# Kernel tuning notes

Hardware: AMD Instinct MI355X
Metric: run time of the kernel (lower is better)

The kernel has to match this reference:

```python
import jax, jax.numpy as jnp
import numpy as np

BH, N, D, M = 64, 8192, 64, 32


def _gaussian_orthogonal_random_matrix(nb_rows, nb_cols, rng):
    # faithful to torch version with scaling=0: QR-orthogonal rows scaled by
    # row norms of a gaussian matrix
    blocks = []
    rows_left = nb_rows
    while rows_left > 0:
        q, _ = np.linalg.qr(rng.standard_normal((nb_cols, nb_cols)))
        blocks.append(q.T[: min(rows_left, nb_cols)])
        rows_left -= nb_cols
    final = np.concatenate(blocks, axis=0)[:nb_rows]
    multiplier = np.linalg.norm(rng.standard_normal((nb_rows, nb_cols)), axis=1)
    return (multiplier[:, None] * final).astype(np.float32)


def setup_inputs() -> dict:
    key = jax.random.key(0)
    k1, k2, k3 = jax.random.split(key, 3)
    q = jax.random.normal(k1, (BH, N, D), dtype=jnp.float32)
    k = jax.random.normal(k2, (BH, N, D), dtype=jnp.float32)
    v = jax.random.normal(k3, (BH, N, D), dtype=jnp.float32)
    proj = jnp.asarray(_gaussian_orthogonal_random_matrix(M, D, np.random.default_rng(0)))
    return {"q": q, "k": k, "v": v, "proj": proj}


def _softmax_kernel(data, proj, is_query, eps=1e-4):
    d = data.shape[-1]
    data_normalizer = d ** -0.25
    ratio = proj.shape[0] ** -0.5
    # [bh, n, m] random-feature logits
    data_dash = jnp.einsum('bnd,md->bnm', data_normalizer * data, proj)
    diag = (0.5 * data_normalizer ** 2) * jnp.sum(data * data, axis=-1, keepdims=True)
    if is_query:
        mx = jnp.max(data_dash, axis=-1, keepdims=True)  # per-row max
    else:
        mx = jnp.max(data_dash)  # global max (as in torch.max(t) with no dim)
    return ratio * (jnp.exp(data_dash - diag - mx) + eps)


def reference(q, k, v, proj):
    qp = _softmax_kernel(q, proj, is_query=True)   # [bh, n, m]
    kp = _softmax_kernel(k, proj, is_query=False)  # [bh, n, m]
    # linear attention: k^T v aggregation then query contraction
    kv = jnp.einsum('bnm,bnd->bmd', kp, v)         # [bh, m, d]
    ksum = jnp.sum(kp, axis=1)                     # [bh, m]
    num = jnp.einsum('bnm,bmd->bnd', qp, kv)       # [bh, n, d]
    den = jnp.einsum('bnm,bm->bn', qp, ksum)       # [bh, n]
    return num / den[..., None]
```

## Files before the change

kernel.cpp:

```cpp
#include <hip/hip_runtime.h>
#include <math.h>

#define BH 64
#define NN 8192
#define DD 64
#define MM 32

#define NROWS (BH*NN)
#define NORMC 0.35355339059327379f
#define RATIO 0.17677669529663689f
#define EPSK  1e-4f
#define DIAGC 0.0625f

#define CPB 64
#define CHUNK 128
#define K12_BLOCKS (BH*CPB)

typedef __attribute__((ext_vector_type(8))) short short8;
typedef __attribute__((ext_vector_type(4))) float f32x4;

union FragU { uint4 u; short8 s; };

__device__ __forceinline__ unsigned bf16r(float x) {
  unsigned u = __float_as_uint(x);
  return (u + 0x7fffu + ((u >> 16) & 1u)) >> 16;
}
__device__ __forceinline__ void cvt8(const float* f, FragU& hi, FragU& lo) {
  unsigned h[8], lw[8];
  #pragma unroll
  for (int j = 0; j < 8; ++j) {
    h[j] = bf16r(f[j]);
    lw[j] = bf16r(f[j] - __uint_as_float(h[j] << 16));
  }
  hi.u = make_uint4(h[0]|(h[1]<<16),  h[2]|(h[3]<<16),  h[4]|(h[5]<<16),  h[6]|(h[7]<<16));
  lo.u = make_uint4(lw[0]|(lw[1]<<16), lw[2]|(lw[3]<<16), lw[4]|(lw[5]<<16), lw[6]|(lw[7]<<16));
}

#define MFMA(a,b,c) __builtin_amdgcn_mfma_f32_16x16x32_bf16((a),(b),(c),0,0,0)

__device__ __forceinline__ float wave_max(float v) {
  #pragma unroll
  for (int off = 32; off > 0; off >>= 1)
    v = fmaxf(v, __shfl_down(v, off, 64));
  return v;
}

__global__ void kfrag_proj(const float* __restrict__ proj,
                           uint4* __restrict__ pfH, uint4* __restrict__ pfL)
{
  const int t = threadIdx.x;
  const int l = t & 63, g = t >> 6;
  const int mt = g >> 1, ks = g & 1;
  const int lr = l & 15, lg = l >> 4;
  float f[8];
  #pragma unroll
  for (int j = 0; j < 8; ++j)
    f[j] = proj[(mt*16 + lr)*DD + ks*32 + lg*8 + j];
  FragU hi, lo; cvt8(f, hi, lo);
  pfH[g*64 + l] = hi.u;
  pfL[g*64 + l] = lo.u;
}

__global__ __launch_bounds__(256, 4) void k12_kv(
    const float* __restrict__ k, const float* __restrict__ v,
    const uint4* __restrict__ pfH, const uint4* __restrict__ pfL,
    float* __restrict__ kvPart, float* __restrict__ ksPart,
    float* __restrict__ vsPart, float* __restrict__ partialMax)
{
  __shared__ float red[8192];
  __shared__ float wmaxL[4];
  const int t = threadIdx.x;
  const int w = t >> 6, l = t & 63;
  const int lr = l & 15, lg = l >> 4;
  const int blk = blockIdx.x;
  const int b = blk >> 6, c = blk & (CPB - 1);
  const size_t nrow0 = (size_t)b * NN + (size_t)c * CHUNK + (size_t)w * 32;

  ushort* eh = (ushort*)red + w * 2560;
  ushort* el = eh + 1280;

  f32x4 accK[2][4];
  #pragma unroll
  for (int mt = 0; mt < 2; ++mt)
    #pragma unroll
    for (int dt = 0; dt < 4; ++dt)
      accK[mt][dt] = (f32x4){0.f, 0.f, 0.f, 0.f};
  float ksacc0 = 0.f, ksacc1 = 0.f;
  float vsum[4] = {0.f, 0.f, 0.f, 0.f};
  float tmax = -3.4e38f;

  #pragma unroll
  for (int rt = 0; rt < 2; ++rt) {
    float sq = 0.f;
    f32x4 a0 = {0.f,0.f,0.f,0.f}, a1 = {0.f,0.f,0.f,0.f};
    #pragma unroll
    for (int ks = 0; ks < 2; ++ks) {
      const float4* src = (const float4*)(k + (nrow0 + rt*16 + lr)*DD + ks*32 + lg*8);
      float4 x0 = src[0], x1 = src[1];
      float qv[8] = {x0.x,x0.y,x0.z,x0.w, x1.x,x1.y,x1.z,x1.w};
      #pragma unroll
      for (int j = 0; j < 8; ++j) sq += qv[j]*qv[j];
      FragU aH, aL; cvt8(qv, aH, aL);

      uintptr_t pfh_ = (uintptr_t)pfH, pfl_ = (uintptr_t)pfL;
      asm volatile("" : "+s"(pfh_), "+s"(pfl_));
      const uint4* pH = (const uint4*)pfh_;
      const uint4* pL = (const uint4*)pfl_;
      FragU pH0, pH1, pL0, pL1;
      pH0.u = pH[ks*64 + l];
      pH1.u = pH[(2+ks)*64 + l];
      pL0.u = pL[ks*64 + l];
      pL1.u = pL[(2+ks)*64 + l];

      a0 = MFMA(aL.s, pH0.s, a0);
      a0 = MFMA(aH.s, pL0.s, a0);
      a0 = MFMA(aH.s, pH0.s, a0);
      a1 = MFMA(aL.s, pH1.s, a1);
      a1 = MFMA(aH.s, pL1.s, a1);
      a1 = MFMA(aH.s, pH1.s, a1);
    }
    sq += __shfl_xor(sq, 16, 64);
    sq += __shfl_xor(sq, 32, 64);
    unsigned h0w[4], l0w[4], h1w[4], l1w[4];
    #pragma unroll
    for (int reg = 0; reg < 4; ++reg) {
      const float diag = DIAGC * __shfl(sq, lg*4 + reg, 64);
      const float d0 = a0[reg] * NORMC;
      const float d1 = a1[reg] * NORMC;
      tmax = fmaxf(tmax, fmaxf(d0, d1));
      const float e0 = __expf(d0 - diag);
      const float e1 = __expf(d1 - diag);
      ksacc0 += e0;
      ksacc1 += e1;
      h0w[reg] = bf16r(e0);
      l0w[reg] = bf16r(e0 - __uint_as_float(h0w[reg] << 16));
      h1w[reg] = bf16r(e1);
      l1w[reg] = bf16r(e1 - __uint_as_float(h1w[reg] << 16));
    }
    const int nloc = rt*16 + lg*4;
    *(unsigned*)(eh + lr*40      + nloc)     = h0w[0] | (h0w[1] << 16);
    *(unsigned*)(eh + lr*40      + nloc + 2) = h0w[2] | (h0w[3] << 16);
    *(unsigned*)(el + lr*40      + nloc)     = l0w[0] | (l0w[1] << 16);
    *(unsigned*)(el + lr*40      + nloc + 2) = l0w[2] | (l0w[3] << 16);
    *(unsigned*)(eh + (lr+16)*40 + nloc)     = h1w[0] | (h1w[1] << 16);
    *(unsigned*)(eh + (lr+16)*40 + nloc + 2) = h1w[2] | (h1w[3] << 16);
    *(unsigned*)(el + (lr+16)*40 + nloc)     = l1w[0] | (l1w[1] << 16);
    *(unsigned*)(el + (lr+16)*40 + nloc + 2) = l1w[2] | (l1w[3] << 16);
  }

  #pragma unroll
  for (int dt = 0; dt < 4; ++dt) {
    float vv[8];
    #pragma unroll
    for (int j = 0; j < 8; ++j)
      vv[j] = v[(nrow0 + lg*8 + j)*DD + dt*16 + lr];
    vsum[dt] += vv[0]+vv[1]+vv[2]+vv[3]+vv[4]+vv[5]+vv[6]+vv[7];
    FragU bHv, bLv; cvt8(vv, bHv, bLv);
    #pragma unroll
    for (int mt = 0; mt < 2; ++mt) {
      FragU aHk, aLk;
      aHk.u = *(const uint4*)(eh + (mt*16 + lr)*40 + lg*8);
      aLk.u = *(const uint4*)(el + (mt*16 + lr)*40 + lg*8);
      accK[mt][dt] = MFMA(aLk.s, bHv.s, accK[mt][dt]);
      accK[mt][dt] = MFMA(aHk.s, bLv.s, accK[mt][dt]);
      accK[mt][dt] = MFMA(aHk.s, bHv.s, accK[mt][dt]);
    }
  }

  tmax = wave_max(tmax);
  if (l == 0) wmaxL[w] = tmax;
  ksacc0 += __shfl_xor(ksacc0, 16, 64);
  ksacc0 += __shfl_xor(ksacc0, 32, 64);
  ksacc1 += __shfl_xor(ksacc1, 16, 64);
  ksacc1 += __shfl_xor(ksacc1, 32, 64);
  #pragma unroll
  for (int dt = 0; dt < 4; ++dt) {
    vsum[dt] += __shfl_xor(vsum[dt], 16, 64);
    vsum[dt] += __shfl_xor(vsum[dt], 32, 64);
  }
  __syncthreads();
  #pragma unroll
  for (int mt = 0; mt < 2; ++mt)
    #pragma unroll
    for (int dt = 0; dt < 4; ++dt)
      #pragma unroll
      for (int reg = 0; reg < 4; ++reg)
        red[((mt*16 + lg*4 + reg)*64 + dt*16 + lr)*4 + w] = accK[mt][dt][reg];
  __syncthreads();
  if (t == 0)
    partialMax[blk] = fmaxf(fmaxf(wmaxL[0], wmaxL[1]), fmaxf(wmaxL[2], wmaxL[3]));
  #pragma unroll
  for (int ii = 0; ii < 8; ++ii) {
    const int o = t + 256 * ii;
    const float4 r4 = *(const float4*)&red[o*4];
    kvPart[(size_t)blk * 2048 + o] = r4.x + r4.y + r4.z + r4.w;
  }
  __syncthreads();
  if (l < 16) {
    red[w*32 + lr]        = ksacc0;
    red[w*32 + 16 + lr]   = ksacc1;
    #pragma unroll
    for (int dt = 0; dt < 4; ++dt)
      red[128 + w*64 + dt*16 + lr] = vsum[dt];
  }
  __syncthreads();
  if (t < 32)
    ksPart[blk*32 + t] = red[t] + red[32+t] + red[64+t] + red[96+t];
  if (t < 64)
    vsPart[blk*64 + t] = red[128+t] + red[192+t] + red[256+t] + red[320+t];
}

__global__ __launch_bounds__(256) void k1b_reduce_max(
    const float* __restrict__ partialMax, float* __restrict__ gmax)
{
  const int t = threadIdx.x;
  float mx = -3.4e38f;
  for (int i = t; i < K12_BLOCKS; i += 256) mx = fmaxf(mx, partialMax[i]);
  mx = wave_max(mx);
  __shared__ float wmaxs[4];
  if ((t & 63) == 0) wmaxs[t >> 6] = mx;
  __syncthreads();
  if (t == 0)
    *gmax = fmaxf(fmaxf(wmaxs[0], wmaxs[1]), fmaxf(wmaxs[2], wmaxs[3]));
}

__global__ __launch_bounds__(256) void k2b_sum(
    const float* __restrict__ kvPart, const float* __restrict__ ksPart,
    const float* __restrict__ vsPart, const float* __restrict__ gmaxPtr,
    float* __restrict__ kvF, float* __restrict__ ksF)
{
  __shared__ float vsumL[64];
  const int blk = blockIdx.x;
  const int b = blk >> 3, seg = blk & 7;
  const int t = threadIdx.x;
  const float scale = __expf(-*gmaxPtr);
  if (t < 64) {
    float s = 0.f;
    #pragma unroll 4
    for (int c = 0; c < CPB; ++c)
      s += vsPart[(b * CPB + c) * 64 + t];
    vsumL[t] = s;
  }
  __syncthreads();
  const int o = seg * 256 + t;
  float s = 0.f;
  #pragma unroll 4
  for (int c = 0; c < CPB; ++c)
    s += kvPart[((size_t)(b * CPB + c)) * 2048 + o];
  kvF[b * 2048 + o] = RATIO * (scale * s + EPSK * vsumL[o & 63]);
  if (seg == 0 && t < 32) {
    float ks = 0.f;
    #pragma unroll 4
    for (int c = 0; c < CPB; ++c)
      ks += ksPart[(b * CPB + c) * 32 + t];
    ksF[b * 32 + t] = RATIO * (scale * ks + EPSK * (float)NN);
  }
}

__global__ __launch_bounds__(256) void k2c_frag(
    const float* __restrict__ kvF,
    uint4* __restrict__ kfH, uint4* __restrict__ kfL)
{
  __shared__ float kvL[2048];
  const int b = blockIdx.x, t = threadIdx.x;
  #pragma unroll
  for (int ii = 0; ii < 8; ++ii)
    kvL[t + 256*ii] = kvF[b*2048 + t + 256*ii];
  __syncthreads();
  const int l = t & 63, dt = t >> 6;
  const int lr = l & 15, lg = l >> 4;
  float f[8];
  #pragma unroll
  for (int j = 0; j < 8; ++j)
    f[j] = kvL[(lg*8 + j)*64 + dt*16 + lr];
  FragU hi, lo; cvt8(f, hi, lo);
  kfH[(b*4 + dt)*64 + l] = hi.u;
  kfL[(b*4 + dt)*64 + l] = lo.u;
}

__global__ __launch_bounds__(256, 4) void k3_out(
    const float* __restrict__ q,
    const uint4* __restrict__ pfH, const uint4* __restrict__ pfL,
    const uint4* __restrict__ kfH, const uint4* __restrict__ kfL,
    const float* __restrict__ ksF, float* __restrict__ out)
{
  __shared__ float dashL[256][36];
  __shared__ float ssqL[256][4];
  const int t = threadIdx.x;
  const int w = t >> 6, l = t & 63;
  const int lr = l & 15, lg = l >> 4;
  const int b = blockIdx.x >> 5;
  const size_t rowBase = (size_t)blockIdx.x * 256;
  const int wrb = w * 64;

  FragU pbH[2][2], pbL[2][2];
  #pragma unroll
  for (int mt = 0; mt < 2; ++mt)
    #pragma unroll
    for (int ks = 0; ks < 2; ++ks) {
      pbH[mt][ks].u = pfH[(mt*2+ks)*64 + l];
      pbL[mt][ks].u = pfL[(mt*2+ks)*64 + l];
    }

  #pragma unroll
  for (int rt = 0; rt < 4; ++rt) {
    const int rrow = wrb + rt*16 + lr;
    f32x4 acc0 = {0.f,0.f,0.f,0.f}, acc1 = {0.f,0.f,0.f,0.f};
    float sq = 0.f;
    #pragma unroll
    for (int ks = 0; ks < 2; ++ks) {
      const float4* src = (const float4*)(q + (rowBase + rrow)*DD + ks*32 + lg*8);
      float4 a0 = src[0], a1 = src[1];
      float qv[8] = {a0.x,a0.y,a0.z,a0.w, a1.x,a1.y,a1.z,a1.w};
      #pragma unroll
      for (int j = 0; j < 8; ++j) sq += qv[j]*qv[j];
      FragU aH, aL; cvt8(qv, aH, aL);
      acc0 = MFMA(aL.s, pbH[0][ks].s, acc0);
      acc0 = MFMA(aH.s, pbL[0][ks].s, acc0);
      acc0 = MFMA(aH.s, pbH[0][ks].s, acc0);
      acc1 = MFMA(aL.s, pbH[1][ks].s, acc1);
      acc1 = MFMA(aH.s, pbL[1][ks].s, acc1);
      acc1 = MFMA(aH.s, pbH[1][ks].s, acc1);
    }
    ssqL[rrow][lg] = sq;
    #pragma unroll
    for (int reg = 0; reg < 4; ++reg) {
      dashL[wrb + rt*16 + lg*4 + reg][lr]      = acc0[reg];
      dashL[wrb + rt*16 + lg*4 + reg][16 + lr] = acc1[reg];
    }
  }

  {
    float dv[32];
    const float4* dr = (const float4*)&dashL[t][0];
    #pragma unroll
    for (int i = 0; i < 8; ++i) {
      float4 v4 = dr[i];
      dv[4*i]=v4.x; dv[4*i+1]=v4.y; dv[4*i+2]=v4.z; dv[4*i+3]=v4.w;
    }
    const float ssq = ssqL[t][0]+ssqL[t][1]+ssqL[t][2]+ssqL[t][3];
    float mx = -3.4e38f;
    #pragma unroll
    for (int m = 0; m < MM; ++m) { dv[m] *= NORMC; mx = fmaxf(mx, dv[m]); }
    const float sub = DIAGC * ssq + mx;
    const float* __restrict__ ksb = ksF + b * 32;
    float den = 0.f;
    #pragma unroll
    for (int m = 0; m < MM; ++m) {
      dv[m] = RATIO * (__expf(dv[m] - sub) + EPSK);
      den = fmaf(dv[m], ksb[m], den);
    }
    const float inv = 1.0f / den;
    unsigned hiw[16], low[16];
    #pragma unroll
    for (int u = 0; u < 16; ++u) {
      const float x0 = dv[2*u] * inv, x1 = dv[2*u+1] * inv;
      const unsigned h0 = bf16r(x0);
      const unsigned l0 = bf16r(x0 - __uint_as_float(h0 << 16));
      const unsigned h1 = bf16r(x1);
      const unsigned l1 = bf16r(x1 - __uint_as_float(h1 << 16));
      hiw[u] = h0 | (h1 << 16);
      low[u] = l0 | (l1 << 16);
    }
    uint4* pr = (uint4*)&dashL[t][0];
    pr[0] = make_uint4(hiw[0],hiw[1],hiw[2],hiw[3]);
    pr[1] = make_uint4(hiw[4],hiw[5],hiw[6],hiw[7]);
    pr[2] = make_uint4(hiw[8],hiw[9],hiw[10],hiw[11]);
    pr[3] = make_uint4(hiw[12],hiw[13],hiw[14],hiw[15]);
    pr[4] = make_uint4(low[0],low[1],low[2],low[3]);
    pr[5] = make_uint4(low[4],low[5],low[6],low[7]);
    pr[6] = make_uint4(low[8],low[9],low[10],low[11]);
    pr[7] = make_uint4(low[12],low[13],low[14],low[15]);
  }

  FragU kbH[4], kbL[4];
  #pragma unroll
  for (int dt = 0; dt < 4; ++dt) {
    kbH[dt].u = kfH[(b*4 + dt)*64 + l];
    kbL[dt].u = kfL[(b*4 + dt)*64 + l];
  }
  #pragma unroll
  for (int rt = 0; rt < 4; ++rt) {
    const uint4* pr = (const uint4*)&dashL[wrb + rt*16 + lr][0];
    FragU aH, aL;
    aH.u = pr[lg];
    aL.u = pr[4 + lg];
    #pragma unroll
    for (int dt = 0; dt < 4; ++dt) {
      f32x4 o = {0.f,0.f,0.f,0.f};
      o = MFMA(aL.s, kbH[dt].s, o);
      o = MFMA(aH.s, kbL[dt].s, o);
      o = MFMA(aH.s, kbH[dt].s, o);
      float* ob = out + (rowBase + wrb + rt*16 + lg*4)*DD + dt*16 + lr;
      ob[0]      = o[0];
      ob[DD]     = o[1];
      ob[2*DD]   = o[2];
      ob[3*DD]   = o[3];
    }
  }
}

extern "C" void kernel_launch(void* const* d_in, const int* in_sizes, int n_in,
                              void* d_out, int out_size, void* d_ws, size_t ws_size,
                              hipStream_t stream) {
  const float* q    = (const float*)d_in[0];
  const float* k    = (const float*)d_in[1];
  const float* v    = (const float*)d_in[2];
  const float* proj = (const float*)d_in[3];
  float* out = (float*)d_out;
  float* ws  = (float*)d_ws;

  float*    partialMax = ws;
  float*    gmax       = ws + 4096;
  float*    kvPart     = ws + 8192;
  float*    ksPart     = kvPart + 8388608;
  float*    vsPart     = ksPart + 131072;
  float*    ksF        = vsPart + 262144;
  float*    kvF        = ksF + 2048;
  unsigned* pfH        = (unsigned*)(kvF + 131072);
  unsigned* pfL        = pfH + 1024;
  unsigned* kfH        = pfL + 1024;
  unsigned* kfL        = kfH + 65536;

  kfrag_proj<<<1, 256, 0, stream>>>(proj, (uint4*)pfH, (uint4*)pfL);
  k12_kv<<<K12_BLOCKS, 256, 0, stream>>>(k, v, (uint4*)pfH, (uint4*)pfL,
                                         kvPart, ksPart, vsPart, partialMax);
  k1b_reduce_max<<<1, 256, 0, stream>>>(partialMax, gmax);
  k2b_sum<<<BH*8, 256, 0, stream>>>(kvPart, ksPart, vsPart, gmax, kvF, ksF);
  k2c_frag<<<BH, 256, 0, stream>>>(kvF, (uint4*)kfH, (uint4*)kfL);
  k3_out<<<NROWS / 256, 256, 0, stream>>>(q, (uint4*)pfH, (uint4*)pfL,
                                          (uint4*)kfH, (uint4*)kfL, ksF, out);
}
```

Before: 156.2 us.

## Double the k/v chunk per block to halve partial kv buffers

The k12_kv kernel now runs 512-thread blocks (8 waves) over 256-row chunks instead of 256-thread blocks over 128-row chunks, so there are half as many blocks. Per-block partial kv, ksum, vsum and max outputs are combined in shared memory over 8 waves: the upper four waves add into the lower four waves' slots in a second pass. This halves the partial-result global traffic written by k12 and read by the reduction kernels. The cost is an extra LDS accumulation pass and tighter register limits under launch bounds of 512 threads × 4 blocks.

```diff
diff --git a/kernel.cpp b/kernel.cpp
--- a/kernel.cpp
+++ b/kernel.cpp
@@ -12,8 +12,8 @@
 #define EPSK  1e-4f
 #define DIAGC 0.0625f
 
-#define CPB 64
-#define CHUNK 128
+#define CPB 32
+#define CHUNK 256
 #define K12_BLOCKS (BH*CPB)
 
 typedef __attribute__((ext_vector_type(8))) short short8;
@@ -61,19 +61,18 @@
   pfL[g*64 + l] = lo.u;
 }
 
-__global__ __launch_bounds__(256, 4) void k12_kv(
+__global__ __launch_bounds__(512, 4) void k12_kv(
     const float* __restrict__ k, const float* __restrict__ v,
     const uint4* __restrict__ pfH, const uint4* __restrict__ pfL,
     float* __restrict__ kvPart, float* __restrict__ ksPart,
     float* __restrict__ vsPart, float* __restrict__ partialMax)
 {
-  __shared__ float red[8192];
-  __shared__ float wmaxL[4];
+  __shared__ float red[10240];
   const int t = threadIdx.x;
   const int w = t >> 6, l = t & 63;
   const int lr = l & 15, lg = l >> 4;
   const int blk = blockIdx.x;
-  const int b = blk >> 6, c = blk & (CPB - 1);
+  const int b = blk >> 5, c = blk & (CPB - 1);
   const size_t nrow0 = (size_t)b * NN + (size_t)c * CHUNK + (size_t)w * 32;
 
   ushort* eh = (ushort*)red + w * 2560;
@@ -168,7 +167,6 @@
   }
 
   tmax = wave_max(tmax);
-  if (l == 0) wmaxL[w] = tmax;
   ksacc0 += __shfl_xor(ksacc0, 16, 64);
   ksacc0 += __shfl_xor(ksacc0, 32, 64);
   ksacc1 += __shfl_xor(ksacc1, 16, 64);
@@ -179,19 +177,36 @@
     vsum[dt] += __shfl_xor(vsum[dt], 32, 64);
   }
   __syncthreads();
-  #pragma unroll
-  for (int mt = 0; mt < 2; ++mt)
-    #pragma unroll
-    for (int dt = 0; dt < 4; ++dt)
+  if (w < 4) {
+    #pragma unroll
+    for (int mt = 0; mt < 2; ++mt)
       #pragma unroll
-      for (int reg = 0; reg < 4; ++reg)
-        red[((mt*16 + lg*4 + reg)*64 + dt*16 + lr)*4 + w] = accK[mt][dt][reg];
-  __syncthreads();
-  if (t == 0)
-    partialMax[blk] = fmaxf(fmaxf(wmaxL[0], wmaxL[1]), fmaxf(wmaxL[2], wmaxL[3]));
-  #pragma unroll
-  for (int ii = 0; ii < 8; ++ii) {
-    const int o = t + 256 * ii;
+      for (int dt = 0; dt < 4; ++dt)
+        #pragma unroll
+        for (int reg = 0; reg < 4; ++reg)
+          red[((mt*16 + lg*4 + reg)*64 + dt*16 + lr)*4 + w] = accK[mt][dt][reg];
+  }
+  if (l == 0) red[8192 + w] = tmax;
+  __syncthreads();
+  if (w >= 4) {
+    #pragma unroll
+    for (int mt = 0; mt < 2; ++mt)
+      #pragma unroll
+      for (int dt = 0; dt < 4; ++dt)
+        #pragma unroll
+        for (int reg = 0; reg < 4; ++reg)
+          red[((mt*16 + lg*4 + reg)*64 + dt*16 + lr)*4 + (w-4)] += accK[mt][dt][reg];
+  }
+  __syncthreads();
+  if (t == 0) {
+    float mx = red[8192];
+    #pragma unroll
+    for (int i = 1; i < 8; ++i) mx = fmaxf(mx, red[8192+i]);
+    partialMax[blk] = mx;
+  }
+  #pragma unroll
+  for (int ii = 0; ii < 4; ++ii) {
+    const int o = t + 512 * ii;
     const float4 r4 = *(const float4*)&red[o*4];
     kvPart[(size_t)blk * 2048 + o] = r4.x + r4.y + r4.z + r4.w;
   }
@@ -201,13 +216,21 @@
     red[w*32 + 16 + lr]   = ksacc1;
     #pragma unroll
     for (int dt = 0; dt < 4; ++dt)
-      red[128 + w*64 + dt*16 + lr] = vsum[dt];
-  }
-  __syncthreads();
-  if (t < 32)
-    ksPart[blk*32 + t] = red[t] + red[32+t] + red[64+t] + red[96+t];
-  if (t < 64)
-    vsPart[blk*64 + t] = red[128+t] + red[192+t] + red[256+t] + red[320+t];
+      red[256 + w*64 + dt*16 + lr] = vsum[dt];
+  }
+  __syncthreads();
+  if (t < 32) {
+    float s = 0.f;
+    #pragma unroll
+    for (int ww = 0; ww < 8; ++ww) s += red[ww*32 + t];
+    ksPart[blk*32 + t] = s;
+  }
+  if (t < 64) {
+    float s = 0.f;
+    #pragma unroll
+    for (int ww = 0; ww < 8; ++ww) s += red[256 + ww*64 + t];
+    vsPart[blk*64 + t] = s;
+  }
 }
 
 __global__ __launch_bounds__(256) void k1b_reduce_max(
@@ -411,11 +434,11 @@
   float* ws  = (float*)d_ws;
 
   float*    partialMax = ws;
-  float*    gmax       = ws + 4096;
-  float*    kvPart     = ws + 8192;
-  float*    ksPart     = kvPart + 8388608;
-  float*    vsPart     = ksPart + 131072;
-  float*    ksF        = vsPart + 262144;
+  float*    gmax       = ws + 2048;
+  float*    kvPart     = ws + 4096;
+  float*    ksPart     = kvPart + 4194304;
+  float*    vsPart     = ksPart + 65536;
+  float*    ksF        = vsPart + 131072;
   float*    kvF        = ksF + 2048;
   unsigned* pfH        = (unsigned*)(kvF + 131072);
   unsigned* pfL        = pfH + 1024;
@@ -423,7 +446,7 @@
   unsigned* kfL        = kfH + 65536;
 
   kfrag_proj<<<1, 256, 0, stream>>>(proj, (uint4*)pfH, (uint4*)pfL);
-  k12_kv<<<K12_BLOCKS, 256, 0, stream>>>(k, v, (uint4*)pfH, (uint4*)pfL,
+  k12_kv<<<K12_BLOCKS, 512, 0, stream>>>(k, v, (uint4*)pfH, (uint4*)pfL,
                                          kvPart, ksPart, vsPart, partialMax);
   k1b_reduce_max<<<1, 256, 0, stream>>>(partialMax, gmax);
   k2b_sum<<<BH*8, 256, 0, stream>>>(kvPart, ksPart, vsPart, gmax, kvF, ksF);
```

New measurement: 154.4 us. No clear change (-1.2%).
